# Optimization experiments

Hardware: AMD Instinct MI355X
Metric: run time of the kernel (lower is better)

Reference implementation:

```python
import jax, jax.numpy as jnp
import numpy as np

N = 262144   # total packed tokens
B = 4096     # number of ragged segments
D = 256      # relation_embed_dim
A = 128      # attention_dim


def setup_inputs() -> dict:
    key = jax.random.key(0)
    k1, k2, k3 = jax.random.split(key, 3)
    relation_embeds = jax.random.normal(k1, (N, D), dtype=jnp.float32)
    # ragged segment ends: B-1 random interior end positions + final position N-1
    rng = np.random.default_rng(0)
    ends = np.sort(rng.choice(N - 1, size=B - 1, replace=False))
    ends = np.concatenate([ends, [N - 1]])
    queries_np = np.zeros((N,), dtype=np.int32)
    queries_np[ends] = 1
    queries = jnp.asarray(queries_np)
    # torch nn.Linear weights: [out, in]
    Wq = jax.random.normal(k2, (A, D), dtype=jnp.float32) / np.sqrt(D)
    Wk = jax.random.normal(k3, (A, D), dtype=jnp.float32) / np.sqrt(D)
    return {"relation_embeds": relation_embeds, "queries": queries,
            "num_segments": B, "Wq": Wq, "Wk": Wk}


def reference(relation_embeds, queries, num_segments, Wq, Wk):
    # segment id per token: exclusive cumsum of end markers
    q = queries.astype(jnp.int32)
    seg = jnp.cumsum(q) - q                      # [N] in [0, num_segments)
    ends = jnp.flatnonzero(q, size=num_segments) # [B] last index of each segment
    # per-segment query = Q(last row of segment); per-token key = K(row)
    q_end = relation_embeds[ends] @ Wq.T         # [B, A]
    k = relation_embeds @ Wk.T                   # [N, A]
    logits = jnp.sum(k * q_end[seg], axis=-1)    # [N] dot(Q_seg, K_token)
    # softmax over each ragged segment (dim=0 within segment)
    m = jax.ops.segment_max(logits, seg, num_segments=num_segments)
    ex = jnp.exp(logits - m[seg])
    denom = jax.ops.segment_sum(ex, seg, num_segments=num_segments)
    return ex / denom[seg]                       # [N] concatenated scores
```

## Files before the change

kernel.cpp:

```cpp
#include <hip/hip_runtime.h>
#include <math.h>

constexpr int N = 262144;
constexpr int B = 4096;
constexpr int D = 256;
constexpr int A = 128;

constexpr int CHUNK  = 1024;
constexpr int NCHUNK = N / CHUNK;

__global__ void k_scan_partials(const int* __restrict__ q, int* __restrict__ partials) {
    int t = threadIdx.x;
    int4 v = ((const int4*)q)[blockIdx.x * (CHUNK / 4) + t];
    int s = v.x + v.y + v.z + v.w;
    __shared__ int sm[256];
    sm[t] = s; __syncthreads();
    for (int o = 128; o > 0; o >>= 1) {
        if (t < o) sm[t] += sm[t + o];
        __syncthreads();
    }
    if (t == 0) partials[blockIdx.x] = sm[0];
}

__global__ void k_scan_offsets(const int* __restrict__ partials, int* __restrict__ offs) {
    int t = threadIdx.x;
    __shared__ int sm[256];
    int v = partials[t];
    sm[t] = v; __syncthreads();
    for (int o = 1; o < 256; o <<= 1) {
        int add = (t >= o) ? sm[t - o] : 0;
        __syncthreads();
        sm[t] += add;
        __syncthreads();
    }
    offs[t] = sm[t] - v;
}

__global__ void k_seg_ends(const int* __restrict__ q, const int* __restrict__ offs,
                           int* __restrict__ seg, int* __restrict__ ends) {
    int t = threadIdx.x;
    int4 v = ((const int4*)q)[blockIdx.x * (CHUNK / 4) + t];
    int tsum = v.x + v.y + v.z + v.w;
    __shared__ int sm[256];
    sm[t] = tsum; __syncthreads();
    for (int o = 1; o < 256; o <<= 1) {
        int add = (t >= o) ? sm[t - o] : 0;
        __syncthreads();
        sm[t] += add;
        __syncthreads();
    }
    int run = offs[blockIdx.x] + sm[t] - tsum;
    int base_idx = blockIdx.x * CHUNK + t * 4;
    int qq[4] = {v.x, v.y, v.z, v.w};
#pragma unroll
    for (int k = 0; k < 4; k++) {
        int idx = base_idx + k;
        seg[idx] = run;
        if (qq[k]) { ends[run] = idx; run++; }
    }
}

__global__ void k_compute_M(const float* __restrict__ Wq, const float* __restrict__ Wk,
                            float* __restrict__ M) {
    int d2 = threadIdx.x;
    int d1 = blockIdx.x;
    float acc = 0.f;
#pragma unroll 4
    for (int a = 0; a < A; a++) {
        acc += Wk[a * D + d1] * Wq[a * D + d2];
    }
    M[d1 * D + d2] = acc;
}

__global__ void k_compute_V(const float* __restrict__ X, const int* __restrict__ ends,
                            const float* __restrict__ M, float* __restrict__ V) {
    int b = blockIdx.x;
    int t = threadIdx.x;
    __shared__ float xs[D];
    int e = ends[b];
    xs[t] = X[(size_t)e * D + t];
    __syncthreads();
    const float4* Mrow = (const float4*)(M + t * D);
    const float4* xv = (const float4*)xs;
    float acc = 0.f;
#pragma unroll 8
    for (int j = 0; j < D / 4; j++) {
        float4 m4 = Mrow[j];
        float4 x4 = xv[j];
        acc += m4.x * x4.x + m4.y * x4.y + m4.z * x4.z + m4.w * x4.w;
    }
    V[b * D + t] = acc;
}

__global__ void k_logits(const float* __restrict__ X, const int* __restrict__ seg,
                         const float* __restrict__ V, float* __restrict__ logits) {
    int wave = threadIdx.x >> 6;
    int lane = threadIdx.x & 63;
    int tok = blockIdx.x * 4 + wave;
    float4 x4 = ((const float4*)(X + (size_t)tok * D))[lane];
    int s = seg[tok];
    float4 v4 = ((const float4*)(V + (size_t)s * D))[lane];
    float p = x4.x * v4.x + x4.y * v4.y + x4.z * v4.z + x4.w * v4.w;
#pragma unroll
    for (int o = 32; o > 0; o >>= 1) p += __shfl_xor(p, o, 64);
    if (lane == 0) logits[tok] = p;
}

__global__ void k_softmax(const float* __restrict__ logits, const int* __restrict__ ends,
                          float* __restrict__ out) {
    int wave = threadIdx.x >> 6;
    int lane = threadIdx.x & 63;
    int b = blockIdx.x * 4 + wave;
    int start = (b == 0) ? 0 : (ends[b - 1] + 1);
    int end = ends[b];
    float m = -INFINITY;
    for (int i = start + lane; i <= end; i += 64) m = fmaxf(m, logits[i]);
#pragma unroll
    for (int o = 32; o > 0; o >>= 1) m = fmaxf(m, __shfl_xor(m, o, 64));
    float ssum = 0.f;
    for (int i = start + lane; i <= end; i += 64) ssum += __expf(logits[i] - m);
#pragma unroll
    for (int o = 32; o > 0; o >>= 1) ssum += __shfl_xor(ssum, o, 64);
    float r = 1.f / ssum;
    for (int i = start + lane; i <= end; i += 64) out[i] = __expf(logits[i] - m) * r;
}

extern "C" void kernel_launch(void* const* d_in, const int* in_sizes, int n_in,
                              void* d_out, int out_size, void* d_ws, size_t ws_size,
                              hipStream_t stream) {
    const float* X  = (const float*)d_in[0];
    const int*   q  = (const int*)d_in[1];
    const float* Wq = (const float*)d_in[3];
    const float* Wk = (const float*)d_in[4];
    float* out = (float*)d_out;

    char* ws = (char*)d_ws;
    size_t off = 0;
    auto alloc = [&](size_t bytes) -> char* {
        char* p = ws + off;
        off += (bytes + 255) & ~(size_t)255;
        return p;
    };
    int*   seg      = (int*)alloc((size_t)N * 4);
    int*   ends     = (int*)alloc((size_t)B * 4);
    int*   partials = (int*)alloc((size_t)NCHUNK * 4);
    int*   offs     = (int*)alloc((size_t)NCHUNK * 4);
    float* M        = (float*)alloc((size_t)D * D * 4);
    float* V        = (float*)alloc((size_t)B * D * 4);
    float* logits   = (float*)alloc((size_t)N * 4);

    k_scan_partials<<<NCHUNK, 256, 0, stream>>>(q, partials);
    k_scan_offsets<<<1, 256, 0, stream>>>(partials, offs);
    k_seg_ends<<<NCHUNK, 256, 0, stream>>>(q, offs, seg, ends);
    k_compute_M<<<D, 256, 0, stream>>>(Wq, Wk, M);
    k_compute_V<<<B, 256, 0, stream>>>(X, ends, M, V);
    k_logits<<<N / 4, 256, 0, stream>>>(X, seg, V, logits);
    k_softmax<<<B / 4, 256, 0, stream>>>(logits, ends, out);
}
```

Measured before the change: 492.0 us.

## Merge scan and M kernels, batch V rows per block, use online softmax

Several changes land together. The partial-sum scan and the Wk^T·Wq product now run in one launch, and the offset scan is folded redundantly into every seg_ends block, which cuts two launches. compute_V now handles 8 segments per block so each M row is read once for 8 query rows. Softmax switches to a single-pass online max/sum, dropping one read of the logits. The costs are redundant scan work in each block, more registers in compute_V, and extra exp calls in the online softmax.

```diff
diff --git a/kernel.cpp b/kernel.cpp
--- a/kernel.cpp
+++ b/kernel.cpp
@@ -1,5 +1,6 @@
 #include <hip/hip_runtime.h>
 #include <math.h>
+#include <float.h>
 
 constexpr int N = 262144;
 constexpr int B = 4096;
@@ -8,49 +9,56 @@
 
 constexpr int CHUNK  = 1024;
 constexpr int NCHUNK = N / CHUNK;
+constexpr int SEGB   = 8;
 
-__global__ void k_scan_partials(const int* __restrict__ q, int* __restrict__ partials) {
+__global__ void k_partials_M(const int* __restrict__ q, int* __restrict__ partials,
+                             const float* __restrict__ Wq, const float* __restrict__ Wk,
+                             float* __restrict__ M) {
     int t = threadIdx.x;
-    int4 v = ((const int4*)q)[blockIdx.x * (CHUNK / 4) + t];
-    int s = v.x + v.y + v.z + v.w;
+    if (blockIdx.x < NCHUNK) {
+        int4 v = ((const int4*)q)[blockIdx.x * (CHUNK / 4) + t];
+        int s = v.x + v.y + v.z + v.w;
+        __shared__ int sm[256];
+        sm[t] = s; __syncthreads();
+        for (int o = 128; o > 0; o >>= 1) {
+            if (t < o) sm[t] += sm[t + o];
+            __syncthreads();
+        }
+        if (t == 0) partials[blockIdx.x] = sm[0];
+    } else {
+        int d1 = blockIdx.x - NCHUNK;
+        int d2 = t;
+        float acc = 0.f;
+#pragma unroll 4
+        for (int a = 0; a < A; a++) {
+            acc = fmaf(Wk[a * D + d1], Wq[a * D + d2], acc);
+        }
+        M[d1 * D + d2] = acc;
+    }
+}
+
+__global__ void k_seg_ends(const int* __restrict__ q, const int* __restrict__ partials,
+                           int* __restrict__ seg, int* __restrict__ ends) {
+    int t = threadIdx.x;
+    int bid = blockIdx.x;
+    __shared__ int sp[256];
     __shared__ int sm[256];
-    sm[t] = s; __syncthreads();
-    for (int o = 128; o > 0; o >>= 1) {
-        if (t < o) sm[t] += sm[t + o];
+    sp[t] = partials[t];
+    int4 v = ((const int4*)q)[bid * (CHUNK / 4) + t];
+    int tsum = v.x + v.y + v.z + v.w;
+    sm[t] = tsum;
+    __syncthreads();
+    for (int o = 1; o < 256; o <<= 1) {
+        int a1 = (t >= o) ? sp[t - o] : 0;
+        int a2 = (t >= o) ? sm[t - o] : 0;
+        __syncthreads();
+        sp[t] += a1;
+        sm[t] += a2;
         __syncthreads();
     }
-    if (t == 0) partials[blockIdx.x] = sm[0];
-}
-
-__global__ void k_scan_offsets(const int* __restrict__ partials, int* __restrict__ offs) {
-    int t = threadIdx.x;
-    __shared__ int sm[256];
-    int v = partials[t];
-    sm[t] = v; __syncthreads();
-    for (int o = 1; o < 256; o <<= 1) {
-        int add = (t >= o) ? sm[t - o] : 0;
-        __syncthreads();
-        sm[t] += add;
-        __syncthreads();
-    }
-    offs[t] = sm[t] - v;
-}
-
-__global__ void k_seg_ends(const int* __restrict__ q, const int* __restrict__ offs,
-                           int* __restrict__ seg, int* __restrict__ ends) {
-    int t = threadIdx.x;
-    int4 v = ((const int4*)q)[blockIdx.x * (CHUNK / 4) + t];
-    int tsum = v.x + v.y + v.z + v.w;
-    __shared__ int sm[256];
-    sm[t] = tsum; __syncthreads();
-    for (int o = 1; o < 256; o <<= 1) {
-        int add = (t >= o) ? sm[t - o] : 0;
-        __syncthreads();
-        sm[t] += add;
-        __syncthreads();
-    }
-    int run = offs[blockIdx.x] + sm[t] - tsum;
-    int base_idx = blockIdx.x * CHUNK + t * 4;
+    int offs = (bid == 0) ? 0 : sp[bid - 1];
+    int run = offs + sm[t] - tsum;
+    int base_idx = bid * CHUNK + t * 4;
     int qq[4] = {v.x, v.y, v.z, v.w};
 #pragma unroll
     for (int k = 0; k < 4; k++) {
@@ -60,36 +68,31 @@
     }
 }
 
-__global__ void k_compute_M(const float* __restrict__ Wq, const float* __restrict__ Wk,
-                            float* __restrict__ M) {
-    int d2 = threadIdx.x;
-    int d1 = blockIdx.x;
-    float acc = 0.f;
-#pragma unroll 4
-    for (int a = 0; a < A; a++) {
-        acc += Wk[a * D + d1] * Wq[a * D + d2];
-    }
-    M[d1 * D + d2] = acc;
-}
-
 __global__ void k_compute_V(const float* __restrict__ X, const int* __restrict__ ends,
                             const float* __restrict__ M, float* __restrict__ V) {
-    int b = blockIdx.x;
     int t = threadIdx.x;
-    __shared__ float xs[D];
-    int e = ends[b];
-    xs[t] = X[(size_t)e * D + t];
-    __syncthreads();
+    int b0 = blockIdx.x * SEGB;
+    const float4* xr[SEGB];
+#pragma unroll
+    for (int r = 0; r < SEGB; r++) {
+        xr[r] = (const float4*)(X + (size_t)ends[b0 + r] * D);
+    }
     const float4* Mrow = (const float4*)(M + t * D);
-    const float4* xv = (const float4*)xs;
-    float acc = 0.f;
-#pragma unroll 8
+    float acc[SEGB];
+#pragma unroll
+    for (int r = 0; r < SEGB; r++) acc[r] = 0.f;
+#pragma unroll 4
     for (int j = 0; j < D / 4; j++) {
         float4 m4 = Mrow[j];
-        float4 x4 = xv[j];
-        acc += m4.x * x4.x + m4.y * x4.y + m4.z * x4.z + m4.w * x4.w;
+#pragma unroll
+        for (int r = 0; r < SEGB; r++) {
+            float4 x4 = xr[r][j];
+            acc[r] = fmaf(m4.x, x4.x, fmaf(m4.y, x4.y,
+                     fmaf(m4.z, x4.z, fmaf(m4.w, x4.w, acc[r]))));
+        }
     }
-    V[b * D + t] = acc;
+#pragma unroll
+    for (int r = 0; r < SEGB; r++) V[(size_t)(b0 + r) * D + t] = acc[r];
 }
 
 __global__ void k_logits(const float* __restrict__ X, const int* __restrict__ seg,
@@ -100,7 +103,7 @@
     float4 x4 = ((const float4*)(X + (size_t)tok * D))[lane];
     int s = seg[tok];
     float4 v4 = ((const float4*)(V + (size_t)s * D))[lane];
-    float p = x4.x * v4.x + x4.y * v4.y + x4.z * v4.z + x4.w * v4.w;
+    float p = fmaf(x4.x, v4.x, fmaf(x4.y, v4.y, fmaf(x4.z, v4.z, x4.w * v4.w)));
 #pragma unroll
     for (int o = 32; o > 0; o >>= 1) p += __shfl_xor(p, o, 64);
     if (lane == 0) logits[tok] = p;
@@ -113,15 +116,22 @@
     int b = blockIdx.x * 4 + wave;
     int start = (b == 0) ? 0 : (ends[b - 1] + 1);
     int end = ends[b];
-    float m = -INFINITY;
-    for (int i = start + lane; i <= end; i += 64) m = fmaxf(m, logits[i]);
+    float m = -FLT_MAX, s = 0.f;
+    for (int i = start + lane; i <= end; i += 64) {
+        float x = logits[i];
+        float nm = fmaxf(m, x);
+        s = s * __expf(m - nm) + __expf(x - nm);
+        m = nm;
+    }
 #pragma unroll
-    for (int o = 32; o > 0; o >>= 1) m = fmaxf(m, __shfl_xor(m, o, 64));
-    float ssum = 0.f;
-    for (int i = start + lane; i <= end; i += 64) ssum += __expf(logits[i] - m);
-#pragma unroll
-    for (int o = 32; o > 0; o >>= 1) ssum += __shfl_xor(ssum, o, 64);
-    float r = 1.f / ssum;
+    for (int o = 32; o > 0; o >>= 1) {
+        float mo = __shfl_xor(m, o, 64);
+        float so = __shfl_xor(s, o, 64);
+        float nm = fmaxf(m, mo);
+        s = s * __expf(m - nm) + so * __expf(mo - nm);
+        m = nm;
+    }
+    float r = 1.f / s;
     for (int i = start + lane; i <= end; i += 64) out[i] = __expf(logits[i] - m) * r;
 }
 
@@ -144,16 +154,13 @@
     int*   seg      = (int*)alloc((size_t)N * 4);
     int*   ends     = (int*)alloc((size_t)B * 4);
     int*   partials = (int*)alloc((size_t)NCHUNK * 4);
-    int*   offs     = (int*)alloc((size_t)NCHUNK * 4);
     float* M        = (float*)alloc((size_t)D * D * 4);
     float* V        = (float*)alloc((size_t)B * D * 4);
     float* logits   = (float*)alloc((size_t)N * 4);
 
-    k_scan_partials<<<NCHUNK, 256, 0, stream>>>(q, partials);
-    k_scan_offsets<<<1, 256, 0, stream>>>(partials, offs);
-    k_seg_ends<<<NCHUNK, 256, 0, stream>>>(q, offs, seg, ends);
-    k_compute_M<<<D, 256, 0, stream>>>(Wq, Wk, M);
-    k_compute_V<<<B, 256, 0, stream>>>(X, ends, M, V);
+    k_partials_M<<<NCHUNK + D, 256, 0, stream>>>(q, partials, Wq, Wk, M);
+    k_seg_ends<<<NCHUNK, 256, 0, stream>>>(q, partials, seg, ends);
+    k_compute_V<<<B / SEGB, 256, 0, stream>>>(X, ends, M, V);
     k_logits<<<N / 4, 256, 0, stream>>>(X, seg, V, logits);
     k_softmax<<<B / 4, 256, 0, stream>>>(logits, ends, out);
 }
```

Result: faster. 413.8 us (-15.9%).
